# Kernel tuning notes

Hardware: AMD Instinct MI355X
Metric: run time of the kernel (lower is better)

Reference implementation:

```python
import jax, jax.numpy as jnp
import numpy as np

EMBED_DIM = 512
NUM_HEADS = 8
HEAD_DIM = EMBED_DIM // NUM_HEADS
SCALE = HEAD_DIM ** -0.5


def setup_inputs() -> dict:
    key = jax.random.key(0)
    ks = jax.random.split(key, 12)
    B, Nq, Nk, C = 2, 2048, 2048, EMBED_DIM
    # xavier_uniform bound for square CxC weights
    bound = float(np.sqrt(6.0 / (C + C)))
    def w(k):
        return jax.random.uniform(k, (C, C), jnp.float32, -bound, bound)
    return {
        "query": jax.random.normal(ks[0], (B, Nq, C), jnp.float32),
        "key": jax.random.normal(ks[1], (B, Nk, C), jnp.float32),
        "value": jax.random.normal(ks[2], (B, Nk, C), jnp.float32),
        "key_padding_mask": jnp.zeros((B, Nk), dtype=bool),
        "Wq": w(ks[3]), "bq": jnp.zeros((C,), jnp.float32),
        "Wk": w(ks[4]), "bk": jnp.zeros((C,), jnp.float32),
        "Wv": w(ks[5]), "bv": jnp.zeros((C,), jnp.float32),
        "Wo": w(ks[6]), "bo": jnp.zeros((C,), jnp.float32),
    }


def reference(query, key, value, key_padding_mask, Wq, bq, Wk, bk, Wv, bv, Wo, bo):
    B, Nq, C = query.shape
    Nk = key.shape[1]
    H, D = NUM_HEADS, HEAD_DIM
    # torch Linear: x @ W.T + b
    Q = (query @ Wq.T + bq).reshape(B, Nq, H, D).transpose(0, 2, 1, 3)  # (B,H,Nq,D)
    K = (key @ Wk.T + bk).reshape(B, Nk, H, D).transpose(0, 2, 1, 3)
    V = (value @ Wv.T + bv).reshape(B, Nk, H, D).transpose(0, 2, 1, 3)
    scores = jnp.einsum("bhqd,bhkd->bhqk", Q, K) * SCALE  # (B,H,Nq,Nk)
    scores = jnp.where(key_padding_mask[:, None, None, :], -jnp.inf, scores)
    attn = jax.nn.softmax(scores, axis=-1)
    out = jnp.einsum("bhqk,bhkd->bhqd", attn, V)  # (B,H,Nq,D)
    out = out.transpose(0, 2, 1, 3).reshape(B, Nq, C)
    return out @ Wo.T + bo
```

## Files before the change

kernel.cpp:

```cpp
#include <hip/hip_runtime.h>

typedef unsigned short u16;
typedef __attribute__((ext_vector_type(8))) short short8;
typedef __attribute__((ext_vector_type(8))) __bf16 bf16x8;
typedef __attribute__((ext_vector_type(4))) float f32x4;
typedef __attribute__((ext_vector_type(4))) unsigned int u32x4;

#define MFMA_BF16(a, b, c) __builtin_amdgcn_mfma_f32_16x16x32_bf16((a), (b), (c), 0, 0, 0)

__device__ __forceinline__ u16 f2bf(float f) {
    unsigned u = __builtin_bit_cast(unsigned, f);
    u += 0x7FFFu + ((u >> 16) & 1u);
    return (u16)(u >> 16);
}

__device__ __forceinline__ unsigned cvt_pk_bf16(float lo, float hi) {
    unsigned r;
    asm("v_cvt_pk_bf16_f32 %0, %1, %2" : "=v"(r) : "v"(lo), "v"(hi));
    return r;
}

__device__ __forceinline__ float fast_exp2(float x) {
    float r;
    asm("v_exp_f32 %0, %1" : "=v"(r) : "v"(x));
    return r;
}

__global__ __launch_bounds__(256) void proj_gemm(
    const float* __restrict__ Xq, const float* __restrict__ Xk, const float* __restrict__ Xv,
    const float* __restrict__ Wq, const float* __restrict__ Wk, const float* __restrict__ Wv,
    const float* __restrict__ bq, const float* __restrict__ bk, const float* __restrict__ bv,
    u16* __restrict__ Oq, u16* __restrict__ Ok, u16* __restrict__ Ov)
{
    constexpr int K = 512, N = 512;
    const int z = blockIdx.z;
    const float* __restrict__ X = (z == 0) ? Xq : (z == 1) ? Xk : Xv;
    const float* __restrict__ W = (z == 0) ? Wq : (z == 1) ? Wk : Wv;
    const float* __restrict__ bias = (z == 0) ? bq : (z == 1) ? bk : bv;
    u16* __restrict__ O = (z == 0) ? Oq : (z == 1) ? Ok : Ov;
    const float alpha = (z == 0) ? 0.125f * 1.44269504088896f : 1.0f;

    __shared__ u16 lA[128 * 64];
    __shared__ u16 lB[128 * 64];

    const int tid = threadIdx.x, lane = tid & 63, w = tid >> 6;
    const int wr = w >> 1, wc = w & 1;
    const int bm = blockIdx.x, bn = blockIdx.y;
    const int r0 = tid >> 3, cc = tid & 7;

    f32x4 acc[4][4];
    for (int m = 0; m < 4; ++m)
        for (int n = 0; n < 4; ++n)
            acc[m][n] = f32x4{0.f, 0.f, 0.f, 0.f};

    for (int kt = 0; kt < K; kt += 64) {
        __syncthreads();
        for (int p = 0; p < 4; ++p) {
            int r = r0 + p * 32;
            {
                const float4* g = (const float4*)(X + (size_t)(bm * 128 + r) * K + kt + cc * 8);
                float4 f0 = g[0], f1 = g[1];
                short8 v;
                v[0] = (short)f2bf(f0.x); v[1] = (short)f2bf(f0.y);
                v[2] = (short)f2bf(f0.z); v[3] = (short)f2bf(f0.w);
                v[4] = (short)f2bf(f1.x); v[5] = (short)f2bf(f1.y);
                v[6] = (short)f2bf(f1.z); v[7] = (short)f2bf(f1.w);
                *(short8*)&lA[r * 64 + ((cc ^ (r & 7)) << 3)] = v;
            }
            {
                const float4* g = (const float4*)(W + (size_t)(bn * 128 + r) * K + kt + cc * 8);
                float4 f0 = g[0], f1 = g[1];
                short8 v;
                v[0] = (short)f2bf(f0.x); v[1] = (short)f2bf(f0.y);
                v[2] = (short)f2bf(f0.z); v[3] = (short)f2bf(f0.w);
                v[4] = (short)f2bf(f1.x); v[5] = (short)f2bf(f1.y);
                v[6] = (short)f2bf(f1.z); v[7] = (short)f2bf(f1.w);
                *(short8*)&lB[r * 64 + ((cc ^ (r & 7)) << 3)] = v;
            }
        }
        __syncthreads();
        for (int kk = 0; kk < 2; ++kk) {
            bf16x8 af[4], bfr[4];
            for (int m = 0; m < 4; ++m) {
                int row = wr * 64 + m * 16 + (lane & 15);
                af[m] = *(const bf16x8*)&lA[row * 64 + (((kk * 4 + (lane >> 4)) ^ (row & 7)) << 3)];
            }
            for (int n = 0; n < 4; ++n) {
                int row = wc * 64 + n * 16 + (lane & 15);
                bfr[n] = *(const bf16x8*)&lB[row * 64 + (((kk * 4 + (lane >> 4)) ^ (row & 7)) << 3)];
            }
            for (int m = 0; m < 4; ++m)
                for (int n = 0; n < 4; ++n)
                    acc[m][n] = MFMA_BF16(af[m], bfr[n], acc[m][n]);
        }
    }
    for (int m = 0; m < 4; ++m)
        for (int n = 0; n < 4; ++n) {
            int row = bm * 128 + wr * 64 + m * 16 + ((lane >> 4) << 2);
            int col = bn * 128 + wc * 64 + n * 16 + (lane & 15);
            float bv_ = bias[col];
            for (int i = 0; i < 4; ++i) {
                float v = (acc[m][n][i] + bv_) * alpha;
                O[(size_t)(row + i) * N + col] = f2bf(v);
            }
        }
}

__global__ __launch_bounds__(256) void out_gemm(
    const u16* __restrict__ A, const float* __restrict__ W,
    const float* __restrict__ bias, float* __restrict__ O)
{
    constexpr int K = 512, N = 512;
    __shared__ u16 lA[128 * 64];
    __shared__ u16 lB[128 * 64];

    const int tid = threadIdx.x, lane = tid & 63, w = tid >> 6;
    const int wr = w >> 1, wc = w & 1;
    const int bm = blockIdx.x, bn = blockIdx.y;
    const int r0 = tid >> 3, cc = tid & 7;

    f32x4 acc[4][4];
    for (int m = 0; m < 4; ++m)
        for (int n = 0; n < 4; ++n)
            acc[m][n] = f32x4{0.f, 0.f, 0.f, 0.f};

    for (int kt = 0; kt < K; kt += 64) {
        __syncthreads();
        for (int p = 0; p < 4; ++p) {
            int r = r0 + p * 32;
            *(short8*)&lA[r * 64 + ((cc ^ (r & 7)) << 3)] =
                *(const short8*)(A + (size_t)(bm * 128 + r) * K + kt + cc * 8);
            const float4* g = (const float4*)(W + (size_t)(bn * 128 + r) * K + kt + cc * 8);
            float4 f0 = g[0], f1 = g[1];
            short8 v;
            v[0] = (short)f2bf(f0.x); v[1] = (short)f2bf(f0.y);
            v[2] = (short)f2bf(f0.z); v[3] = (short)f2bf(f0.w);
            v[4] = (short)f2bf(f1.x); v[5] = (short)f2bf(f1.y);
            v[6] = (short)f2bf(f1.z); v[7] = (short)f2bf(f1.w);
            *(short8*)&lB[r * 64 + ((cc ^ (r & 7)) << 3)] = v;
        }
        __syncthreads();
        for (int kk = 0; kk < 2; ++kk) {
            bf16x8 af[4], bfr[4];
            for (int m = 0; m < 4; ++m) {
                int row = wr * 64 + m * 16 + (lane & 15);
                af[m] = *(const bf16x8*)&lA[row * 64 + (((kk * 4 + (lane >> 4)) ^ (row & 7)) << 3)];
            }
            for (int n = 0; n < 4; ++n) {
                int row = wc * 64 + n * 16 + (lane & 15);
                bfr[n] = *(const bf16x8*)&lB[row * 64 + (((kk * 4 + (lane >> 4)) ^ (row & 7)) << 3)];
            }
            for (int m = 0; m < 4; ++m)
                for (int n = 0; n < 4; ++n)
                    acc[m][n] = MFMA_BF16(af[m], bfr[n], acc[m][n]);
        }
    }
    for (int m = 0; m < 4; ++m)
        for (int n = 0; n < 4; ++n) {
            int row = bm * 128 + wr * 64 + m * 16 + ((lane >> 4) << 2);
            int col = bn * 128 + wc * 64 + n * 16 + (lane & 15);
            float bv_ = bias[col];
            for (int i = 0; i < 4; ++i)
                O[(size_t)(row + i) * N + col] = acc[m][n][i] + bv_;
        }
}

__global__ __launch_bounds__(256) void attn_k(
    const u16* __restrict__ Qp, const u16* __restrict__ Kp, const u16* __restrict__ Vp,
    const unsigned char* __restrict__ mask, u16* __restrict__ Ob)
{
    constexpr int C = 512, NK = 2048, NP = NK / 128;
    __shared__ u16 lK[2][2][64 * 64];
    __shared__ u16 lV[2][2][64 * 64];

    const int tid = threadIdx.x, lane = tid & 63, w = tid >> 6;
    const int gd = lane >> 4, q15 = lane & 15;
    const int bh = blockIdx.x, qb = blockIdx.y;
    const int b = bh >> 3, h = bh & 7;
    const size_t qrow0 = (size_t)b * 2048 + qb * 64;
    const size_t krow0 = (size_t)b * 2048;
    const int col0 = h * 64;
    const int rs = tid >> 3, cc = tid & 7;

    bf16x8 qf[2];
    {
        const u16* qrow = Qp + (qrow0 + w * 16 + q15) * C + col0;
        qf[0] = *(const bf16x8*)(qrow + gd * 8);
        qf[1] = *(const bf16x8*)(qrow + 32 + gd * 8);
    }

    float mst = -1e30f, lstp = 0.f;
    f32x4 oacc[4];
    #pragma unroll
    for (int i = 0; i < 4; ++i) oacc[i] = f32x4{0.f, 0.f, 0.f, 0.f};

    {
        short8 kr[2][2], vr[2][2];
        #pragma unroll
        for (int u = 0; u < 2; ++u)
            #pragma unroll
            for (int p = 0; p < 2; ++p) {
                int r = rs + p * 32;
                kr[u][p] = *(const short8*)(Kp + (krow0 + u * 64 + r) * C + col0 + cc * 8);
                vr[u][p] = *(const short8*)(Vp + (krow0 + u * 64 + r) * C + col0 + cc * 8);
            }
        #pragma unroll
        for (int u = 0; u < 2; ++u)
            #pragma unroll
            for (int p = 0; p < 2; ++p) {
                int r = rs + p * 32;
                *(short8*)&lK[0][u][r * 64 + ((cc ^ (r & 7)) << 3)] = kr[u][p];
                #pragma unroll
                for (int j = 0; j < 8; ++j)
                    lV[0][u][(cc * 8 + j) * 64 + (((r >> 3) ^ ((j + cc) & 7)) << 3) + (r & 7)] = (u16)vr[u][p][j];
            }
    }
    __syncthreads();

    int cur = 0;
    for (int pj = 0; pj < NP; ++pj) {
        const int kv = pj * 128;
        const bool hasnext = (pj + 1 < NP);
        short8 kreg[2][2], vreg[2][2];
        if (hasnext) {
            #pragma unroll
            for (int u = 0; u < 2; ++u)
                #pragma unroll
                for (int p = 0; p < 2; ++p) {
                    int r = rs + p * 32;
                    kreg[u][p] = *(const short8*)(Kp + (krow0 + kv + 128 + u * 64 + r) * C + col0 + cc * 8);
                    vreg[u][p] = *(const short8*)(Vp + (krow0 + kv + 128 + u * 64 + r) * C + col0 + cc * 8);
                }
        }
        unsigned char mby[2];
        mby[0] = mask[(size_t)b * NK + kv + lane];
        mby[1] = mask[(size_t)b * NK + kv + 64 + lane];

        f32x4 s2[2][4];
        #pragma unroll
        for (int u = 0; u < 2; ++u)
            #pragma unroll
            for (int i = 0; i < 4; ++i) s2[u][i] = f32x4{0.f, 0.f, 0.f, 0.f};
        __builtin_amdgcn_s_setprio(1);
        #pragma unroll
        for (int u = 0; u < 2; ++u) {
            const u16* Kc = &lK[cur][u][0];
            #pragma unroll
            for (int kb = 0; kb < 2; ++kb)
                #pragma unroll
                for (int t4 = 0; t4 < 4; ++t4) {
                    int krow = t4 * 16 + q15;
                    bf16x8 kf = *(const bf16x8*)&Kc[krow * 64 + (((kb * 4 + gd) ^ (krow & 7)) << 3)];
                    s2[u][t4] = MFMA_BF16(kf, qf[kb], s2[u][t4]);
                }
        }
        __builtin_amdgcn_s_setprio(0);

        #pragma unroll
        for (int u = 0; u < 2; ++u) {
            unsigned long long m64 = __ballot(mby[u] != 0);
            if (m64) {
                #pragma unroll
                for (int t4 = 0; t4 < 4; ++t4)
                    #pragma unroll
                    for (int i = 0; i < 4; ++i) {
                        int k = t4 * 16 + gd * 4 + i;
                        if ((m64 >> k) & 1ull) s2[u][t4][i] = -1e30f;
                    }
            }

            float pmax = s2[u][0][0];
            #pragma unroll
            for (int t4 = 0; t4 < 4; ++t4)
                #pragma unroll
                for (int i = 0; i < 4; ++i) pmax = fmaxf(pmax, s2[u][t4][i]);

            if (!__all(pmax - mst <= 11.0f)) {
                float rm = fmaxf(pmax, __shfl_xor(pmax, 16));
                rm = fmaxf(rm, __shfl_xor(rm, 32));
                float mn = fmaxf(mst, rm);
                float sf = exp2f(mst - mn);
                mst = mn;
                lstp *= sf;
                #pragma unroll
                for (int i = 0; i < 4; ++i) {
                    float sfi = __shfl(sf, (lane & 48) | ((gd << 2) + i));
                    #pragma unroll
                    for (int t2 = 0; t2 < 4; ++t2) oacc[t2][i] *= sfi;
                }
            }

            float p[4][4];
            float rsum = 0.f;
            #pragma unroll
            for (int t4 = 0; t4 < 4; ++t4)
                #pragma unroll
                for (int i = 0; i < 4; ++i) {
                    float e = fast_exp2(s2[u][t4][i] - mst);
                    p[t4][i] = e;
                    rsum += e;
                }
            lstp += rsum;

            const u16* Vc = &lV[cur][u][0];
            __builtin_amdgcn_s_setprio(1);
            #pragma unroll
            for (int kb = 0; kb < 2; ++kb) {
                u32x4 pw;
                pw[0] = cvt_pk_bf16(p[2 * kb][0], p[2 * kb][1]);
                pw[1] = cvt_pk_bf16(p[2 * kb][2], p[2 * kb][3]);
                pw[2] = cvt_pk_bf16(p[2 * kb + 1][0], p[2 * kb + 1][1]);
                pw[3] = cvt_pk_bf16(p[2 * kb + 1][2], p[2 * kb + 1][3]);
                bf16x8 pa = __builtin_bit_cast(bf16x8, pw);
                #pragma unroll
                for (int t2 = 0; t2 < 4; ++t2) {
                    int d = t2 * 16 + q15;
                    int swd = (d + (d >> 3)) & 7;
                    int base = d * 64 + 4 * (gd & 1);
                    uint2 v0 = *(const uint2*)&Vc[base + (((4 * kb + 0 + (gd >> 1)) ^ swd) << 3)];
                    uint2 v1 = *(const uint2*)&Vc[base + (((4 * kb + 2 + (gd >> 1)) ^ swd) << 3)];
                    u32x4 vw; vw[0] = v0.x; vw[1] = v0.y; vw[2] = v1.x; vw[3] = v1.y;
                    bf16x8 vf = __builtin_bit_cast(bf16x8, vw);
                    oacc[t2] = MFMA_BF16(pa, vf, oacc[t2]);
                }
            }
            __builtin_amdgcn_s_setprio(0);
        }

        if (hasnext) {
            int nxt = cur ^ 1;
            #pragma unroll
            for (int u = 0; u < 2; ++u)
                #pragma unroll
                for (int p = 0; p < 2; ++p) {
                    int r = rs + p * 32;
                    *(short8*)&lK[nxt][u][r * 64 + ((cc ^ (r & 7)) << 3)] = kreg[u][p];
                    #pragma unroll
                    for (int j = 0; j < 8; ++j)
                        lV[nxt][u][(cc * 8 + j) * 64 + (((r >> 3) ^ ((j + cc) & 7)) << 3) + (r & 7)] = (u16)vreg[u][p][j];
                }
            __syncthreads();
            cur = nxt;
        }
    }

    float lsum = lstp + __shfl_xor(lstp, 16);
    lsum += __shfl_xor(lsum, 32);

    #pragma unroll
    for (int i = 0; i < 4; ++i) {
        float li = __shfl(lsum, (lane & 48) | ((gd << 2) + i));
        float inv = 1.f / li;
        int qg = qb * 64 + w * 16 + gd * 4 + i;
        #pragma unroll
        for (int t2 = 0; t2 < 4; ++t2) {
            int col = col0 + t2 * 16 + q15;
            Ob[((size_t)b * 2048 + qg) * C + col] = f2bf(oacc[t2][i] * inv);
        }
    }
}

extern "C" void kernel_launch(void* const* d_in, const int* in_sizes, int n_in,
                              void* d_out, int out_size, void* d_ws, size_t ws_size,
                              hipStream_t stream) {
    const float* query = (const float*)d_in[0];
    const float* key   = (const float*)d_in[1];
    const float* value = (const float*)d_in[2];
    const unsigned char* mask = (const unsigned char*)d_in[3];
    const float* Wq = (const float*)d_in[4];
    const float* bq = (const float*)d_in[5];
    const float* Wk = (const float*)d_in[6];
    const float* bk = (const float*)d_in[7];
    const float* Wv = (const float*)d_in[8];
    const float* bv = (const float*)d_in[9];
    const float* Wo = (const float*)d_in[10];
    const float* bo = (const float*)d_in[11];

    u16* ws = (u16*)d_ws;
    u16* Qp = ws;
    u16* Kp = ws + 2097152;
    u16* Vp = ws + 4194304;
    u16* Ob = ws + 6291456;

    dim3 gp(32, 4, 3);
    proj_gemm<<<gp, 256, 0, stream>>>(query, key, value, Wq, Wk, Wv, bq, bk, bv, Qp, Kp, Vp);

    dim3 ga(16, 32);
    attn_k<<<ga, 256, 0, stream>>>(Qp, Kp, Vp, mask, Ob);

    dim3 go(32, 4);
    out_gemm<<<go, 256, 0, stream>>>(Ob, Wo, bo, (float*)d_out);
}
```

Before: 72.37 us.

## Split KV range across two wave groups per block and merge partial softmax

```diff
diff --git a/kernel.cpp b/kernel.cpp
--- a/kernel.cpp
+++ b/kernel.cpp
@@ -165,15 +165,16 @@
         }
 }
 
-__global__ __launch_bounds__(256) void attn_k(
+__global__ __launch_bounds__(512, 4) void attn_k(
     const u16* __restrict__ Qp, const u16* __restrict__ Kp, const u16* __restrict__ Vp,
     const unsigned char* __restrict__ mask, u16* __restrict__ Ob)
 {
-    constexpr int C = 512, NK = 2048, NP = NK / 128;
+    constexpr int C = 512, NK = 2048, KVH = 1024, NP = KVH / 128;
     __shared__ u16 lK[2][2][64 * 64];
     __shared__ u16 lV[2][2][64 * 64];
 
     const int tid = threadIdx.x, lane = tid & 63, w = tid >> 6;
+    const int g = w >> 2, wg = w & 3;
     const int gd = lane >> 4, q15 = lane & 15;
     const int bh = blockIdx.x, qb = blockIdx.y;
     const int b = bh >> 3, h = bh & 7;
@@ -184,7 +185,7 @@
 
     bf16x8 qf[2];
     {
-        const u16* qrow = Qp + (qrow0 + w * 16 + q15) * C + col0;
+        const u16* qrow = Qp + (qrow0 + wg * 16 + q15) * C + col0;
         qf[0] = *(const bf16x8*)(qrow + gd * 8);
         qf[1] = *(const bf16x8*)(qrow + 32 + gd * 8);
     }
@@ -194,47 +195,41 @@
     #pragma unroll
     for (int i = 0; i < 4; ++i) oacc[i] = f32x4{0.f, 0.f, 0.f, 0.f};
 
-    {
-        short8 kr[2][2], vr[2][2];
-        #pragma unroll
-        for (int u = 0; u < 2; ++u)
-            #pragma unroll
-            for (int p = 0; p < 2; ++p) {
-                int r = rs + p * 32;
-                kr[u][p] = *(const short8*)(Kp + (krow0 + u * 64 + r) * C + col0 + cc * 8);
-                vr[u][p] = *(const short8*)(Vp + (krow0 + u * 64 + r) * C + col0 + cc * 8);
-            }
-        #pragma unroll
-        for (int u = 0; u < 2; ++u)
-            #pragma unroll
-            for (int p = 0; p < 2; ++p) {
-                int r = rs + p * 32;
-                *(short8*)&lK[0][u][r * 64 + ((cc ^ (r & 7)) << 3)] = kr[u][p];
+    short8 kreg[2][2], vreg[2][2];
+    #pragma unroll
+    for (int g2 = 0; g2 < 2; ++g2)
+        #pragma unroll
+        for (int u = 0; u < 2; ++u) {
+            kreg[g2][u] = *(const short8*)(Kp + (krow0 + g2 * KVH + u * 64 + rs) * C + col0 + cc * 8);
+            vreg[g2][u] = *(const short8*)(Vp + (krow0 + g2 * KVH + u * 64 + rs) * C + col0 + cc * 8);
+        }
+
+    for (int pj = 0; pj < NP; ++pj) {
+        #pragma unroll
+        for (int g2 = 0; g2 < 2; ++g2)
+            #pragma unroll
+            for (int u = 0; u < 2; ++u) {
+                *(short8*)&lK[g2][u][rs * 64 + ((cc ^ (rs & 7)) << 3)] = kreg[g2][u];
                 #pragma unroll
                 for (int j = 0; j < 8; ++j)
-                    lV[0][u][(cc * 8 + j) * 64 + (((r >> 3) ^ ((j + cc) & 7)) << 3) + (r & 7)] = (u16)vr[u][p][j];
-            }
-    }
-    __syncthreads();
-
-    int cur = 0;
-    for (int pj = 0; pj < NP; ++pj) {
-        const int kv = pj * 128;
-        const bool hasnext = (pj + 1 < NP);
-        short8 kreg[2][2], vreg[2][2];
-        if (hasnext) {
-            #pragma unroll
-            for (int u = 0; u < 2; ++u)
-                #pragma unroll
-                for (int p = 0; p < 2; ++p) {
-                    int r = rs + p * 32;
-                    kreg[u][p] = *(const short8*)(Kp + (krow0 + kv + 128 + u * 64 + r) * C + col0 + cc * 8);
-                    vreg[u][p] = *(const short8*)(Vp + (krow0 + kv + 128 + u * 64 + r) * C + col0 + cc * 8);
-                }
-        }
+                    lV[g2][u][(cc * 8 + j) * 64 + (((rs >> 3) ^ ((j + cc) & 7)) << 3) + (rs & 7)] = (u16)vreg[g2][u][j];
+            }
+        if (pj + 1 < NP) {
+            #pragma unroll
+            for (int g2 = 0; g2 < 2; ++g2)
+                #pragma unroll
+                for (int u = 0; u < 2; ++u) {
+                    const size_t row = krow0 + g2 * KVH + (pj + 1) * 128 + u * 64 + rs;
+                    kreg[g2][u] = *(const short8*)(Kp + row * C + col0 + cc * 8);
+                    vreg[g2][u] = *(const short8*)(Vp + row * C + col0 + cc * 8);
+                }
+        }
+        __syncthreads();
+
+        const int kvb = g * KVH + pj * 128;
         unsigned char mby[2];
-        mby[0] = mask[(size_t)b * NK + kv + lane];
-        mby[1] = mask[(size_t)b * NK + kv + 64 + lane];
+        mby[0] = mask[(size_t)b * NK + kvb + lane];
+        mby[1] = mask[(size_t)b * NK + kvb + 64 + lane];
 
         f32x4 s2[2][4];
         #pragma unroll
@@ -244,7 +239,7 @@
         __builtin_amdgcn_s_setprio(1);
         #pragma unroll
         for (int u = 0; u < 2; ++u) {
-            const u16* Kc = &lK[cur][u][0];
+            const u16* Kc = &lK[g][u][0];
             #pragma unroll
             for (int kb = 0; kb < 2; ++kb)
                 #pragma unroll
@@ -302,7 +297,7 @@
                 }
             lstp += rsum;
 
-            const u16* Vc = &lV[cur][u][0];
+            const u16* Vc = &lV[g][u][0];
             __builtin_amdgcn_s_setprio(1);
             #pragma unroll
             for (int kb = 0; kb < 2; ++kb) {
@@ -326,36 +321,40 @@
             }
             __builtin_amdgcn_s_setprio(0);
         }
-
-        if (hasnext) {
-            int nxt = cur ^ 1;
-            #pragma unroll
-            for (int u = 0; u < 2; ++u)
-                #pragma unroll
-                for (int p = 0; p < 2; ++p) {
-                    int r = rs + p * 32;
-                    *(short8*)&lK[nxt][u][r * 64 + ((cc ^ (r & 7)) << 3)] = kreg[u][p];
-                    #pragma unroll
-                    for (int j = 0; j < 8; ++j)
-                        lV[nxt][u][(cc * 8 + j) * 64 + (((r >> 3) ^ ((j + cc) & 7)) << 3) + (r & 7)] = (u16)vreg[u][p][j];
-                }
-            __syncthreads();
-            cur = nxt;
-        }
+        __syncthreads();
     }
 
     float lsum = lstp + __shfl_xor(lstp, 16);
     lsum += __shfl_xor(lsum, 32);
 
-    #pragma unroll
-    for (int i = 0; i < 4; ++i) {
-        float li = __shfl(lsum, (lane & 48) | ((gd << 2) + i));
-        float inv = 1.f / li;
-        int qg = qb * 64 + w * 16 + gd * 4 + i;
-        #pragma unroll
-        for (int t2 = 0; t2 < 4; ++t2) {
-            int col = col0 + t2 * 16 + q15;
-            Ob[((size_t)b * 2048 + qg) * C + col] = f2bf(oacc[t2][i] * inv);
+    float* mrg = (float*)&lK[0][0][0];
+    const int mbase = (wg * 64 + lane) * 18;
+    if (g == 1) {
+        #pragma unroll
+        for (int t2 = 0; t2 < 4; ++t2)
+            #pragma unroll
+            for (int i = 0; i < 4; ++i) mrg[mbase + t2 * 4 + i] = oacc[t2][i];
+        mrg[mbase + 16] = mst;
+        mrg[mbase + 17] = lsum;
+    }
+    __syncthreads();
+    if (g == 0) {
+        float mst1 = mrg[mbase + 16], ls1 = mrg[mbase + 17];
+        float m = fmaxf(mst, mst1);
+        float a0 = exp2f(mst - m), a1 = exp2f(mst1 - m);
+        float lr = lsum * a0 + ls1 * a1;
+        #pragma unroll
+        for (int i = 0; i < 4; ++i) {
+            int srcl = (lane & 48) | ((gd << 2) + i);
+            float a0i = __shfl(a0, srcl), a1i = __shfl(a1, srcl), li = __shfl(lr, srcl);
+            float inv = 1.f / li;
+            int qg = qb * 64 + wg * 16 + gd * 4 + i;
+            #pragma unroll
+            for (int t2 = 0; t2 < 4; ++t2) {
+                float o1 = mrg[mbase + t2 * 4 + i];
+                float vfin = (oacc[t2][i] * a0i + o1 * a1i) * inv;
+                Ob[((size_t)b * 2048 + qg) * C + col0 + t2 * 16 + q15] = f2bf(vfin);
+            }
         }
     }
 }
@@ -386,7 +385,7 @@
     proj_gemm<<<gp, 256, 0, stream>>>(query, key, value, Wq, Wk, Wv, bq, bk, bv, Qp, Kp, Vp);
 
     dim3 ga(16, 32);
-    attn_k<<<ga, 256, 0, stream>>>(Qp, Kp, Vp, mask, Ob);
+    attn_k<<<ga, 512, 0, stream>>>(Qp, Kp, Vp, mask, Ob);
 
     dim3 go(32, 4);
     out_gemm<<<go, 256, 0, stream>>>(Ob, Wo, bo, (float*)d_out);
```

New measurement: 114.1 us. +57.7%, slower.

## Split attention over two KV halves and merge partials inside output GEMM

Applied to the files above, without the earlier changes.

```diff
diff --git a/kernel.cpp b/kernel.cpp
--- a/kernel.cpp
+++ b/kernel.cpp
@@ -12,6 +12,11 @@
     unsigned u = __builtin_bit_cast(unsigned, f);
     u += 0x7FFFu + ((u >> 16) & 1u);
     return (u16)(u >> 16);
+}
+
+__device__ __forceinline__ float bf2f(short s) {
+    unsigned u = ((unsigned)(u16)s) << 16;
+    return __builtin_bit_cast(float, u);
 }
 
 __device__ __forceinline__ unsigned cvt_pk_bf16(float lo, float hi) {
@@ -107,8 +112,9 @@
 }
 
 __global__ __launch_bounds__(256) void out_gemm(
-    const u16* __restrict__ A, const float* __restrict__ W,
-    const float* __restrict__ bias, float* __restrict__ O)
+    const u16* __restrict__ Op0, const u16* __restrict__ Op1,
+    const float2* __restrict__ ml0, const float2* __restrict__ ml1,
+    const float* __restrict__ W, const float* __restrict__ bias, float* __restrict__ O)
 {
     constexpr int K = 512, N = 512;
     __shared__ u16 lA[128 * 64];
@@ -125,19 +131,37 @@
             acc[m][n] = f32x4{0.f, 0.f, 0.f, 0.f};
 
     for (int kt = 0; kt < K; kt += 64) {
+        const int h = kt >> 6;
         __syncthreads();
         for (int p = 0; p < 4; ++p) {
             int r = r0 + p * 32;
-            *(short8*)&lA[r * 64 + ((cc ^ (r & 7)) << 3)] =
-                *(const short8*)(A + (size_t)(bm * 128 + r) * K + kt + cc * 8);
-            const float4* g = (const float4*)(W + (size_t)(bn * 128 + r) * K + kt + cc * 8);
-            float4 f0 = g[0], f1 = g[1];
-            short8 v;
-            v[0] = (short)f2bf(f0.x); v[1] = (short)f2bf(f0.y);
-            v[2] = (short)f2bf(f0.z); v[3] = (short)f2bf(f0.w);
-            v[4] = (short)f2bf(f1.x); v[5] = (short)f2bf(f1.y);
-            v[6] = (short)f2bf(f1.z); v[7] = (short)f2bf(f1.w);
-            *(short8*)&lB[r * 64 + ((cc ^ (r & 7)) << 3)] = v;
+            int grow = bm * 128 + r;
+            {
+                int mli = (((grow >> 11) * 8 + h) << 11) | (grow & 2047);
+                float2 v0 = ml0[mli], v1 = ml1[mli];
+                float m = fmaxf(v0.x, v1.x);
+                float e0 = exp2f(v0.x - m) * v0.y;
+                float e1 = exp2f(v1.x - m) * v1.y;
+                float inv = 1.f / (e0 + e1);
+                float w0 = e0 * inv, w1 = e1 * inv;
+                short8 a0 = *(const short8*)(Op0 + (size_t)grow * K + kt + cc * 8);
+                short8 a1 = *(const short8*)(Op1 + (size_t)grow * K + kt + cc * 8);
+                short8 v;
+                #pragma unroll
+                for (int j = 0; j < 8; ++j)
+                    v[j] = (short)f2bf(bf2f(a0[j]) * w0 + bf2f(a1[j]) * w1);
+                *(short8*)&lA[r * 64 + ((cc ^ (r & 7)) << 3)] = v;
+            }
+            {
+                const float4* g = (const float4*)(W + (size_t)(bn * 128 + r) * K + kt + cc * 8);
+                float4 f0 = g[0], f1 = g[1];
+                short8 v;
+                v[0] = (short)f2bf(f0.x); v[1] = (short)f2bf(f0.y);
+                v[2] = (short)f2bf(f0.z); v[3] = (short)f2bf(f0.w);
+                v[4] = (short)f2bf(f1.x); v[5] = (short)f2bf(f1.y);
+                v[6] = (short)f2bf(f1.z); v[7] = (short)f2bf(f1.w);
+                *(short8*)&lB[r * 64 + ((cc ^ (r & 7)) << 3)] = v;
+            }
         }
         __syncthreads();
         for (int kk = 0; kk < 2; ++kk) {
@@ -165,22 +189,27 @@
         }
 }
 
-__global__ __launch_bounds__(256) void attn_k(
+__global__ __launch_bounds__(256, 4) void attn_k(
     const u16* __restrict__ Qp, const u16* __restrict__ Kp, const u16* __restrict__ Vp,
-    const unsigned char* __restrict__ mask, u16* __restrict__ Ob)
+    const unsigned char* __restrict__ mask,
+    u16* __restrict__ Op0, u16* __restrict__ Op1,
+    float2* __restrict__ ml0, float2* __restrict__ ml1)
 {
-    constexpr int C = 512, NK = 2048, NP = NK / 128;
-    __shared__ u16 lK[2][2][64 * 64];
-    __shared__ u16 lV[2][2][64 * 64];
+    constexpr int C = 512, NK = 2048, KVH = 1024, NP = KVH / 128;
+    __shared__ u16 lK[2][64 * 64];
+    __shared__ u16 lV[2][64 * 64];
 
     const int tid = threadIdx.x, lane = tid & 63, w = tid >> 6;
     const int gd = lane >> 4, q15 = lane & 15;
-    const int bh = blockIdx.x, qb = blockIdx.y;
+    const int bh = blockIdx.x, qb = blockIdx.y, z = blockIdx.z;
     const int b = bh >> 3, h = bh & 7;
     const size_t qrow0 = (size_t)b * 2048 + qb * 64;
-    const size_t krow0 = (size_t)b * 2048;
+    const size_t krow0 = (size_t)b * 2048 + (size_t)z * KVH;
     const int col0 = h * 64;
     const int rs = tid >> 3, cc = tid & 7;
+
+    u16* __restrict__ Op = z ? Op1 : Op0;
+    float2* __restrict__ ml = z ? ml1 : ml0;
 
     bf16x8 qf[2];
     {
@@ -194,47 +223,43 @@
     #pragma unroll
     for (int i = 0; i < 4; ++i) oacc[i] = f32x4{0.f, 0.f, 0.f, 0.f};
 
-    {
-        short8 kr[2][2], vr[2][2];
+    short8 kreg[2][2], vreg[2][2];
+    #pragma unroll
+    for (int u = 0; u < 2; ++u)
+        #pragma unroll
+        for (int p = 0; p < 2; ++p) {
+            int r = rs + p * 32;
+            kreg[u][p] = *(const short8*)(Kp + (krow0 + u * 64 + r) * C + col0 + cc * 8);
+            vreg[u][p] = *(const short8*)(Vp + (krow0 + u * 64 + r) * C + col0 + cc * 8);
+        }
+
+    for (int pj = 0; pj < NP; ++pj) {
+        __syncthreads();
         #pragma unroll
         for (int u = 0; u < 2; ++u)
             #pragma unroll
             for (int p = 0; p < 2; ++p) {
                 int r = rs + p * 32;
-                kr[u][p] = *(const short8*)(Kp + (krow0 + u * 64 + r) * C + col0 + cc * 8);
-                vr[u][p] = *(const short8*)(Vp + (krow0 + u * 64 + r) * C + col0 + cc * 8);
-            }
-        #pragma unroll
-        for (int u = 0; u < 2; ++u)
-            #pragma unroll
-            for (int p = 0; p < 2; ++p) {
-                int r = rs + p * 32;
-                *(short8*)&lK[0][u][r * 64 + ((cc ^ (r & 7)) << 3)] = kr[u][p];
+                *(short8*)&lK[u][r * 64 + ((cc ^ (r & 7)) << 3)] = kreg[u][p];
                 #pragma unroll
                 for (int j = 0; j < 8; ++j)
-                    lV[0][u][(cc * 8 + j) * 64 + (((r >> 3) ^ ((j + cc) & 7)) << 3) + (r & 7)] = (u16)vr[u][p][j];
-            }
-    }
-    __syncthreads();
-
-    int cur = 0;
-    for (int pj = 0; pj < NP; ++pj) {
-        const int kv = pj * 128;
-        const bool hasnext = (pj + 1 < NP);
-        short8 kreg[2][2], vreg[2][2];
-        if (hasnext) {
+                    lV[u][(cc * 8 + j) * 64 + (((r >> 3) ^ ((j + cc) & 7)) << 3) + (r & 7)] = (u16)vreg[u][p][j];
+            }
+        if (pj + 1 < NP) {
             #pragma unroll
             for (int u = 0; u < 2; ++u)
                 #pragma unroll
                 for (int p = 0; p < 2; ++p) {
-                    int r = rs + p * 32;
-                    kreg[u][p] = *(const short8*)(Kp + (krow0 + kv + 128 + u * 64 + r) * C + col0 + cc * 8);
-                    vreg[u][p] = *(const short8*)(Vp + (krow0 + kv + 128 + u * 64 + r) * C + col0 + cc * 8);
+                    const size_t row = krow0 + (pj + 1) * 128 + u * 64 + rs + p * 32;
+                    kreg[u][p] = *(const short8*)(Kp + row * C + col0 + cc * 8);
+                    vreg[u][p] = *(const short8*)(Vp + row * C + col0 + cc * 8);
                 }
         }
+        __syncthreads();
+
         unsigned char mby[2];
-        mby[0] = mask[(size_t)b * NK + kv + lane];
-        mby[1] = mask[(size_t)b * NK + kv + 64 + lane];
+        mby[0] = mask[(size_t)b * NK + z * KVH + pj * 128 + lane];
+        mby[1] = mask[(size_t)b * NK + z * KVH + pj * 128 + 64 + lane];
 
         f32x4 s2[2][4];
         #pragma unroll
@@ -244,7 +269,7 @@
         __builtin_amdgcn_s_setprio(1);
         #pragma unroll
         for (int u = 0; u < 2; ++u) {
-            const u16* Kc = &lK[cur][u][0];
+            const u16* Kc = &lK[u][0];
             #pragma unroll
             for (int kb = 0; kb < 2; ++kb)
                 #pragma unroll
@@ -302,7 +327,7 @@
                 }
             lstp += rsum;
 
-            const u16* Vc = &lV[cur][u][0];
+            const u16* Vc = &lV[u][0];
             __builtin_amdgcn_s_setprio(1);
             #pragma unroll
             for (int kb = 0; kb < 2; ++kb) {
@@ -326,26 +351,13 @@
             }
             __builtin_amdgcn_s_setprio(0);
         }
-
-        if (hasnext) {
-            int nxt = cur ^ 1;
-            #pragma unroll
-            for (int u = 0; u < 2; ++u)
-                #pragma unroll
-                for (int p = 0; p < 2; ++p) {
-                    int r = rs + p * 32;
-                    *(short8*)&lK[nxt][u][r * 64 + ((cc ^ (r & 7)) << 3)] = kreg[u][p];
-                    #pragma unroll
-                    for (int j = 0; j < 8; ++j)
-                        lV[nxt][u][(cc * 8 + j) * 64 + (((r >> 3) ^ ((j + cc) & 7)) << 3) + (r & 7)] = (u16)vreg[u][p][j];
-                }
-            __syncthreads();
-            cur = nxt;
-        }
     }
 
     float lsum = lstp + __shfl_xor(lstp, 16);
     lsum += __shfl_xor(lsum, 32);
+
+    if (gd == 0)
+        ml[bh * 2048 + qb * 64 + w * 16 + q15] = make_float2(mst, lsum);
 
     #pragma unroll
     for (int i = 0; i < 4; ++i) {
@@ -355,7 +367,7 @@
         #pragma unroll
         for (int t2 = 0; t2 < 4; ++t2) {
             int col = col0 + t2 * 16 + q15;
-            Ob[((size_t)b * 2048 + qg) * C + col] = f2bf(oacc[t2][i] * inv);
+            Op[((size_t)b * 2048 + qg) * C + col] = f2bf(oacc[t2][i] * inv);
         }
     }
 }
@@ -377,17 +389,20 @@
     const float* bo = (const float*)d_in[11];
 
     u16* ws = (u16*)d_ws;
-    u16* Qp = ws;
-    u16* Kp = ws + 2097152;
-    u16* Vp = ws + 4194304;
-    u16* Ob = ws + 6291456;
+    u16* Qp  = ws;
+    u16* Kp  = ws + 2097152;
+    u16* Vp  = ws + 4194304;
+    u16* Op0 = ws + 6291456;
+    u16* Op1 = ws + 8388608;
+    float2* ml0 = (float2*)(ws + 10485760);
+    float2* ml1 = (float2*)(ws + 10485760 + 131072);
 
     dim3 gp(32, 4, 3);
     proj_gemm<<<gp, 256, 0, stream>>>(query, key, value, Wq, Wk, Wv, bq, bk, bv, Qp, Kp, Vp);
 
-    dim3 ga(16, 32);
-    attn_k<<<ga, 256, 0, stream>>>(Qp, Kp, Vp, mask, Ob);
+    dim3 ga(16, 32, 2);
+    attn_k<<<ga, 256, 0, stream>>>(Qp, Kp, Vp, mask, Op0, Op1, ml0, ml1);
 
     dim3 go(32, 4);
-    out_gemm<<<go, 256, 0, stream>>>(Ob, Wo, bo, (float*)d_out);
-}
+    out_gemm<<<go, 256, 0, stream>>>(Op0, Op1, ml0, ml1, Wo, bo, (float*)d_out);
+}
```

New measurement: 151.9 us. +109.8%, slower.
